# Kernel optimization log

Measured on AMD Instinct MI355X. Metric: run time of the kernel, lower is better.

The kernel has to match this reference:

```python
import jax, jax.numpy as jnp
import numpy as np

N_NODES = 50000


def _gcn_conv(x, W, b, src, dst, n):
    # PyG GCNConv: linear, then D^{-1/2}(A+I)D^{-1/2} aggregation, then bias.
    x = x @ W  # [N, out]
    loops = jnp.arange(n, dtype=src.dtype)
    src_f = jnp.concatenate([src, loops])  # add self-loops
    dst_f = jnp.concatenate([dst, loops])
    deg = jax.ops.segment_sum(jnp.ones_like(dst_f, dtype=x.dtype), dst_f, num_segments=n)
    dinv = jnp.where(deg > 0, jax.lax.rsqrt(deg), 0.0)
    norm = dinv[src_f] * dinv[dst_f]            # [E+N]
    msg = x[src_f] * norm[:, None]              # gather + scale
    out = jax.ops.segment_sum(msg, dst_f, num_segments=n)  # scatter-add
    return out + b


def setup_inputs() -> dict:
    key = jax.random.key(0)
    k1, k2, k3, k4 = jax.random.split(key, 4)
    ninp = 128
    emb = jax.random.normal(k1, (N_NODES, ninp), dtype=jnp.float32)
    emb = emb.at[0].set(0.0)  # padding_idx=0
    W1 = jax.random.normal(k2, (ninp, 2 * ninp), dtype=jnp.float32) * (1.0 / np.sqrt(ninp))
    b1 = jnp.zeros((2 * ninp,), dtype=jnp.float32)
    W2 = jax.random.normal(k3, (2 * ninp, ninp), dtype=jnp.float32) * (1.0 / np.sqrt(2 * ninp))
    b2 = jnp.zeros((ninp,), dtype=jnp.float32)
    edge_index = jax.random.randint(k4, (2, 800000), 0, N_NODES, dtype=jnp.int64)
    return {"emb": emb, "W1": W1, "b1": b1, "W2": W2, "b2": b2, "edge_index": edge_index}


def reference(emb, W1, b1, W2, b2, edge_index) -> jnp.ndarray:
    src, dst = edge_index[0], edge_index[1]
    h = _gcn_conv(emb, W1, b1, src, dst, N_NODES)   # [N, 2*ninp]
    # dropout in eval mode -> identity
    out = _gcn_conv(h, W2, b2, src, dst, N_NODES)   # [N, ninp]
    return out
```

## Files before the change

### kernel.cpp

```cpp
#include <hip/hip_runtime.h>

#define N_NODES 50000
#define N_EDGES 800000
#define NB 196

typedef unsigned int uint;
typedef short bf16x8 __attribute__((ext_vector_type(8)));
typedef float f32x4 __attribute__((ext_vector_type(4)));

__device__ __forceinline__ ushort f2bf(float f) {
    union { float f; uint u; } v; v.f = f;
    uint r = (v.u + 0x7FFFu + ((v.u >> 16) & 1u)) >> 16;
    return (ushort)r;
}
__device__ __forceinline__ float bf_lo(uint u) { return __uint_as_float(u << 16); }
__device__ __forceinline__ float bf_hi(uint u) { return __uint_as_float(u & 0xFFFF0000u); }

__global__ void k_tobf16(const float* __restrict__ in, uint* __restrict__ out) {
    int t = blockIdx.x * 256 + threadIdx.x;
    const float4* i4 = (const float4*)in + (size_t)t * 2;
    float4 v0 = i4[0], v1 = i4[1];
    uint4 o;
    o.x = (uint)f2bf(v0.x) | ((uint)f2bf(v0.y) << 16);
    o.y = (uint)f2bf(v0.z) | ((uint)f2bf(v0.w) << 16);
    o.z = (uint)f2bf(v1.x) | ((uint)f2bf(v1.y) << 16);
    o.w = (uint)f2bf(v1.z) | ((uint)f2bf(v1.w) << 16);
    ((uint4*)out)[t] = o;
}

__global__ void k_w12(const float* __restrict__ W1, const float* __restrict__ W2,
                      const float* __restrict__ b1, ushort* __restrict__ W12t,
                      float* __restrict__ bvec) {
    int n = threadIdx.x;
    int k = blockIdx.x;
    float s = 0.f;
    if (k < 128) {
        for (int m = 0; m < 256; ++m) s = fmaf(W1[(size_t)k * 256 + m], W2[(size_t)m * 128 + n], s);
        W12t[(size_t)n * 128 + k] = f2bf(s);
    } else {
        for (int m = 0; m < 256; ++m) s = fmaf(b1[m], W2[(size_t)m * 128 + n], s);
        bvec[n] = s;
    }
}


__global__ void k_zero(int* counts) {
    int i = blockIdx.x * 256 + threadIdx.x;
    if (i < N_NODES) counts[i] = 0;
}

__global__ void k_histrank(const int* __restrict__ dst, int* __restrict__ counts,
                           ushort* __restrict__ rank) {
    int e = blockIdx.x * 256 + threadIdx.x;
    if (e < N_EDGES) rank[e] = (ushort)atomicAdd(&counts[dst[e]], 1);
}

__global__ void k_blocksum(const int* __restrict__ counts, int* __restrict__ bsum) {
    __shared__ int lds[256];
    int t = threadIdx.x;
    int i = blockIdx.x * 256 + t;
    int v = (i < N_NODES) ? counts[i] : 0;
    lds[t] = v;
    __syncthreads();
    for (int off = 128; off > 0; off >>= 1) {
        if (t < off) lds[t] += lds[t + off];
        __syncthreads();
    }
    if (t == 0) bsum[blockIdx.x] = lds[0];
}

__global__ void k_scanb(const int* __restrict__ bsum, int* __restrict__ boff) {
    __shared__ int lds[256];
    int t = threadIdx.x;
    int v = (t < NB) ? bsum[t] : 0;
    lds[t] = v;
    __syncthreads();
    for (int off = 1; off < 256; off <<= 1) {
        int o = (t >= off) ? lds[t - off] : 0;
        __syncthreads();
        lds[t] += o;
        __syncthreads();
    }
    if (t < NB) boff[t] = lds[t] - v;
}

__global__ void k_scatter_rp(const int* __restrict__ counts, const int* __restrict__ boff,
                             int* __restrict__ row_ptr, float* __restrict__ dinv) {
    __shared__ int lds[256];
    int t = threadIdx.x;
    int i = blockIdx.x * 256 + t;
    int v = (i < N_NODES) ? counts[i] : 0;
    lds[t] = v;
    __syncthreads();
    for (int off = 1; off < 256; off <<= 1) {
        int o = (t >= off) ? lds[t - off] : 0;
        __syncthreads();
        lds[t] += o;
        __syncthreads();
    }
    if (i < N_NODES) {
        row_ptr[i] = boff[blockIdx.x] + lds[t] - v;
        dinv[i] = rsqrtf((float)(v + 1));
    }
    if (i == 0) row_ptr[N_NODES] = N_EDGES;
}

__global__ void k_fillr(const int* __restrict__ src, const int* __restrict__ dst,
                        const ushort* __restrict__ rank, const int* __restrict__ row_ptr,
                        ushort* __restrict__ csr_src) {
    int e = blockIdx.x * 256 + threadIdx.x;
    if (e >= N_EDGES) return;
    int pos = row_ptr[dst[e]] + (int)rank[e];
    csr_src[pos] = (ushort)src[e];
}

template<bool NVEC>
__global__ void k_gather128h(const uint* __restrict__ xh, const ushort* __restrict__ csr,
                             const int* __restrict__ rp, const float* __restrict__ dinv,
                             uint* __restrict__ outp, float* __restrict__ nvec) {
    int node = blockIdx.x * 4 + (threadIdx.x >> 6);
    int lane = threadIdx.x & 63;
    int q = lane >> 4;
    int fl = lane & 15;
    int beg = rp[node], end = rp[node + 1];
    const uint4* xb = (const uint4*)xh;
    float a[8];
    #pragma unroll
    for (int i = 0; i < 8; ++i) a[i] = 0.f;
    float sc = 0.f;

    for (int j = beg + q; j < end; j += 16) {
        int j1 = j + 4, j2 = j + 8, j3 = j + 12;
        int s0 = csr[j];
        int s1 = (j1 < end) ? (int)csr[j1] : s0;
        int s2 = (j2 < end) ? (int)csr[j2] : s0;
        int s3 = (j3 < end) ? (int)csr[j3] : s0;
        float c0 = dinv[s0];
        float c1 = (j1 < end) ? dinv[s1] : 0.f;
        float c2 = (j2 < end) ? dinv[s2] : 0.f;
        float c3 = (j3 < end) ? dinv[s3] : 0.f;
        uint4 u0 = xb[(size_t)s0 * 16 + fl];
        uint4 u1 = xb[(size_t)s1 * 16 + fl];
        uint4 u2 = xb[(size_t)s2 * 16 + fl];
        uint4 u3 = xb[(size_t)s3 * 16 + fl];
        sc += c0 + c1 + c2 + c3;
        a[0] = fmaf(c0, bf_lo(u0.x), a[0]); a[1] = fmaf(c0, bf_hi(u0.x), a[1]);
        a[2] = fmaf(c0, bf_lo(u0.y), a[2]); a[3] = fmaf(c0, bf_hi(u0.y), a[3]);
        a[4] = fmaf(c0, bf_lo(u0.z), a[4]); a[5] = fmaf(c0, bf_hi(u0.z), a[5]);
        a[6] = fmaf(c0, bf_lo(u0.w), a[6]); a[7] = fmaf(c0, bf_hi(u0.w), a[7]);
        a[0] = fmaf(c1, bf_lo(u1.x), a[0]); a[1] = fmaf(c1, bf_hi(u1.x), a[1]);
        a[2] = fmaf(c1, bf_lo(u1.y), a[2]); a[3] = fmaf(c1, bf_hi(u1.y), a[3]);
        a[4] = fmaf(c1, bf_lo(u1.z), a[4]); a[5] = fmaf(c1, bf_hi(u1.z), a[5]);
        a[6] = fmaf(c1, bf_lo(u1.w), a[6]); a[7] = fmaf(c1, bf_hi(u1.w), a[7]);
        a[0] = fmaf(c2, bf_lo(u2.x), a[0]); a[1] = fmaf(c2, bf_hi(u2.x), a[1]);
        a[2] = fmaf(c2, bf_lo(u2.y), a[2]); a[3] = fmaf(c2, bf_hi(u2.y), a[3]);
        a[4] = fmaf(c2, bf_lo(u2.z), a[4]); a[5] = fmaf(c2, bf_hi(u2.z), a[5]);
        a[6] = fmaf(c2, bf_lo(u2.w), a[6]); a[7] = fmaf(c2, bf_hi(u2.w), a[7]);
        a[0] = fmaf(c3, bf_lo(u3.x), a[0]); a[1] = fmaf(c3, bf_hi(u3.x), a[1]);
        a[2] = fmaf(c3, bf_lo(u3.y), a[2]); a[3] = fmaf(c3, bf_hi(u3.y), a[3]);
        a[4] = fmaf(c3, bf_lo(u3.z), a[4]); a[5] = fmaf(c3, bf_hi(u3.z), a[5]);
        a[6] = fmaf(c3, bf_lo(u3.w), a[6]); a[7] = fmaf(c3, bf_hi(u3.w), a[7]);
    }
    #pragma unroll
    for (int off = 16; off < 64; off <<= 1) {
        #pragma unroll
        for (int i = 0; i < 8; ++i) a[i] += __shfl_xor(a[i], off);
        sc += __shfl_xor(sc, off);
    }
    if (q == 0) {
        float dd = dinv[node];
        float dd2 = dd * dd;
        uint4 u = xb[(size_t)node * 16 + fl];
        float s[8] = { bf_lo(u.x), bf_hi(u.x), bf_lo(u.y), bf_hi(u.y),
                       bf_lo(u.z), bf_hi(u.z), bf_lo(u.w), bf_hi(u.w) };
        uint4 p;
        float o0 = fmaf(dd, a[0], dd2 * s[0]), o1 = fmaf(dd, a[1], dd2 * s[1]);
        float o2 = fmaf(dd, a[2], dd2 * s[2]), o3 = fmaf(dd, a[3], dd2 * s[3]);
        float o4 = fmaf(dd, a[4], dd2 * s[4]), o5 = fmaf(dd, a[5], dd2 * s[5]);
        float o6 = fmaf(dd, a[6], dd2 * s[6]), o7 = fmaf(dd, a[7], dd2 * s[7]);
        p.x = (uint)f2bf(o0) | ((uint)f2bf(o1) << 16);
        p.y = (uint)f2bf(o2) | ((uint)f2bf(o3) << 16);
        p.z = (uint)f2bf(o4) | ((uint)f2bf(o5) << 16);
        p.w = (uint)f2bf(o6) | ((uint)f2bf(o7) << 16);
        ((uint4*)outp)[(size_t)node * 16 + fl] = p;
        if (NVEC && fl == 0) nvec[node] = fmaf(dd, sc, dd2);
    }
}

__global__ void __launch_bounds__(256)
k_gemm_out(const ushort* __restrict__ A, const ushort* __restrict__ Wt,
           const float* __restrict__ nvec, const float* __restrict__ bvec,
           const float* __restrict__ b2, float* __restrict__ out) {
    constexpr int K = 128, NC = 128, KC = 4, TPW = 2;
    const int lane = threadIdx.x & 63;
    const int wave = threadIdx.x >> 6;
    const int row0 = blockIdx.x * 16;
    const int r = row0 + (lane & 15);
    const int ksub = (lane >> 4) * 8;

    f32x4 acc[TPW];
    int col[TPW];
    #pragma unroll
    for (int t = 0; t < TPW; ++t) {
        acc[t] = (f32x4){0.f, 0.f, 0.f, 0.f};
        col[t] = (wave * TPW + t) * 16 + (lane & 15);
    }
    #pragma unroll
    for (int kc = 0; kc < KC; ++kc) {
        bf16x8 af = *(const bf16x8*)(A + (size_t)r * K + kc * 32 + ksub);
        #pragma unroll
        for (int t = 0; t < TPW; ++t) {
            bf16x8 bf = *(const bf16x8*)(Wt + (size_t)col[t] * K + kc * 32 + ksub);
            acc[t] = __builtin_amdgcn_mfma_f32_16x16x32_bf16(af, bf, acc[t], 0, 0, 0);
        }
    }
    const int rb = row0 + (lane >> 4) * 4;
    float nv[4];
    #pragma unroll
    for (int e = 0; e < 4; ++e) nv[e] = nvec[rb + e];
    #pragma unroll
    for (int t = 0; t < TPW; ++t) {
        float bv = bvec[col[t]];
        float bb = b2[col[t]];
        #pragma unroll
        for (int e = 0; e < 4; ++e) {
            out[(size_t)(rb + e) * NC + col[t]] = acc[t][e] + nv[e] * bv + bb;
        }
    }
}

extern "C" void kernel_launch(void* const* d_in, const int* in_sizes, int n_in,
                              void* d_out, int out_size, void* d_ws, size_t ws_size,
                              hipStream_t stream) {
    const float* emb = (const float*)d_in[0];
    const float* W1  = (const float*)d_in[1];
    const float* b1  = (const float*)d_in[2];
    const float* W2  = (const float*)d_in[3];
    const float* b2  = (const float*)d_in[4];
    const int*   ei  = (const int*)d_in[5];
    const int* src = ei;
    const int* dst = ei + N_EDGES;

    char* ws = (char*)d_ws;
    float*  dinv    = (float*) (ws);
    int*    counts  = (int*)   (ws + (256ull << 10));
    int*    row_ptr = (int*)   (ws + (512ull << 10));
    int*    bsum    = (int*)   (ws + (768ull << 10));
    int*    boff    = (int*)   (ws + (772ull << 10));
    ushort* rank    = (ushort*)(ws + (1ull << 20));
    ushort* csr_src = (ushort*)(ws + (3ull << 20));
    ushort* W12t    = (ushort*)(ws + (5ull << 20));
    float*  bvec    = (float*) (ws + (5ull << 20) + (64ull << 10));
    float*  nvec    = (float*) (ws + (5ull << 20) + (128ull << 10));
    uint*   emb_h   = (uint*)  (ws + (6ull  << 20));
    uint*   G       = (uint*)  (ws + (19ull << 20));
    uint*   G2      = (uint*)  (ws + (32ull << 20));
    float*  out     = (float*)d_out;

    k_tobf16<<<N_NODES * 128 / 8 / 256, 256, 0, stream>>>(emb, emb_h);
    k_w12<<<129, 128, 0, stream>>>(W1, W2, b1, W12t, bvec);

    k_zero<<<NB, 256, 0, stream>>>(counts);
    k_histrank<<<(N_EDGES + 255) / 256, 256, 0, stream>>>(dst, counts, rank);
    k_blocksum<<<NB, 256, 0, stream>>>(counts, bsum);
    k_scanb<<<1, 256, 0, stream>>>(bsum, boff);
    k_scatter_rp<<<NB, 256, 0, stream>>>(counts, boff, row_ptr, dinv);
    k_fillr<<<(N_EDGES + 255) / 256, 256, 0, stream>>>(src, dst, rank, row_ptr, csr_src);

    k_gather128h<false><<<12500, 256, 0, stream>>>(emb_h, csr_src, row_ptr, dinv, G, nullptr);
    k_gather128h<true><<<12500, 256, 0, stream>>>(G, csr_src, row_ptr, dinv, G2, nvec);
    k_gemm_out<<<N_NODES / 16, 256, 0, stream>>>((const ushort*)G2, W12t, nvec, bvec, b2, out);
}
```

Baseline: 159.9 us.

## Split bf16 features into 16-column chunks and gather each chunk separately

```diff
diff --git a/kernel.cpp b/kernel.cpp
--- a/kernel.cpp
+++ b/kernel.cpp
@@ -16,8 +16,9 @@
 __device__ __forceinline__ float bf_lo(uint u) { return __uint_as_float(u << 16); }
 __device__ __forceinline__ float bf_hi(uint u) { return __uint_as_float(u & 0xFFFF0000u); }
 
-__global__ void k_tobf16(const float* __restrict__ in, uint* __restrict__ out) {
+__global__ void k_tobf16c(const float* __restrict__ in, uint* __restrict__ out) {
     int t = blockIdx.x * 256 + threadIdx.x;
+    int node = t >> 4, part = t & 15;
     const float4* i4 = (const float4*)in + (size_t)t * 2;
     float4 v0 = i4[0], v1 = i4[1];
     uint4 o;
@@ -25,7 +26,8 @@
     o.y = (uint)f2bf(v0.z) | ((uint)f2bf(v0.w) << 16);
     o.z = (uint)f2bf(v1.x) | ((uint)f2bf(v1.y) << 16);
     o.w = (uint)f2bf(v1.z) | ((uint)f2bf(v1.w) << 16);
-    ((uint4*)out)[t] = o;
+    int c8 = part >> 1, half = part & 1;
+    ((uint4*)out)[((size_t)c8 * N_NODES + node) * 2 + half] = o;
 }
 
 __global__ void k_w12(const float* __restrict__ W1, const float* __restrict__ W2,
@@ -115,75 +117,45 @@
 }
 
 template<bool NVEC>
-__global__ void k_gather128h(const uint* __restrict__ xh, const ushort* __restrict__ csr,
-                             const int* __restrict__ rp, const float* __restrict__ dinv,
-                             uint* __restrict__ outp, float* __restrict__ nvec) {
-    int node = blockIdx.x * 4 + (threadIdx.x >> 6);
+__global__ void k_gatherc(const uint* __restrict__ xh, const ushort* __restrict__ csr,
+                          const int* __restrict__ rp, const float* __restrict__ dinv,
+                          uint* __restrict__ outp, float* __restrict__ nvec) {
+    int b = blockIdx.x;
+    int c = b & 7;
+    int node = (b >> 3) * 4 + (threadIdx.x >> 6);
     int lane = threadIdx.x & 63;
-    int q = lane >> 4;
-    int fl = lane & 15;
+    int g = lane >> 3, fl = lane & 7;
     int beg = rp[node], end = rp[node + 1];
-    const uint4* xb = (const uint4*)xh;
-    float a[8];
-    #pragma unroll
-    for (int i = 0; i < 8; ++i) a[i] = 0.f;
-    float sc = 0.f;
-
-    for (int j = beg + q; j < end; j += 16) {
-        int j1 = j + 4, j2 = j + 8, j3 = j + 12;
+    const uint* tb = xh + (size_t)c * N_NODES * 8;
+    float a0 = 0.f, a1 = 0.f, sc = 0.f;
+
+    for (int j = beg + g; j < end; j += 16) {
         int s0 = csr[j];
+        float c0 = dinv[s0];
+        uint u0 = tb[(size_t)s0 * 8 + fl];
+        int j1 = j + 8;
         int s1 = (j1 < end) ? (int)csr[j1] : s0;
-        int s2 = (j2 < end) ? (int)csr[j2] : s0;
-        int s3 = (j3 < end) ? (int)csr[j3] : s0;
-        float c0 = dinv[s0];
         float c1 = (j1 < end) ? dinv[s1] : 0.f;
-        float c2 = (j2 < end) ? dinv[s2] : 0.f;
-        float c3 = (j3 < end) ? dinv[s3] : 0.f;
-        uint4 u0 = xb[(size_t)s0 * 16 + fl];
-        uint4 u1 = xb[(size_t)s1 * 16 + fl];
-        uint4 u2 = xb[(size_t)s2 * 16 + fl];
-        uint4 u3 = xb[(size_t)s3 * 16 + fl];
-        sc += c0 + c1 + c2 + c3;
-        a[0] = fmaf(c0, bf_lo(u0.x), a[0]); a[1] = fmaf(c0, bf_hi(u0.x), a[1]);
-        a[2] = fmaf(c0, bf_lo(u0.y), a[2]); a[3] = fmaf(c0, bf_hi(u0.y), a[3]);
-        a[4] = fmaf(c0, bf_lo(u0.z), a[4]); a[5] = fmaf(c0, bf_hi(u0.z), a[5]);
-        a[6] = fmaf(c0, bf_lo(u0.w), a[6]); a[7] = fmaf(c0, bf_hi(u0.w), a[7]);
-        a[0] = fmaf(c1, bf_lo(u1.x), a[0]); a[1] = fmaf(c1, bf_hi(u1.x), a[1]);
-        a[2] = fmaf(c1, bf_lo(u1.y), a[2]); a[3] = fmaf(c1, bf_hi(u1.y), a[3]);
-        a[4] = fmaf(c1, bf_lo(u1.z), a[4]); a[5] = fmaf(c1, bf_hi(u1.z), a[5]);
-        a[6] = fmaf(c1, bf_lo(u1.w), a[6]); a[7] = fmaf(c1, bf_hi(u1.w), a[7]);
-        a[0] = fmaf(c2, bf_lo(u2.x), a[0]); a[1] = fmaf(c2, bf_hi(u2.x), a[1]);
-        a[2] = fmaf(c2, bf_lo(u2.y), a[2]); a[3] = fmaf(c2, bf_hi(u2.y), a[3]);
-        a[4] = fmaf(c2, bf_lo(u2.z), a[4]); a[5] = fmaf(c2, bf_hi(u2.z), a[5]);
-        a[6] = fmaf(c2, bf_lo(u2.w), a[6]); a[7] = fmaf(c2, bf_hi(u2.w), a[7]);
-        a[0] = fmaf(c3, bf_lo(u3.x), a[0]); a[1] = fmaf(c3, bf_hi(u3.x), a[1]);
-        a[2] = fmaf(c3, bf_lo(u3.y), a[2]); a[3] = fmaf(c3, bf_hi(u3.y), a[3]);
-        a[4] = fmaf(c3, bf_lo(u3.z), a[4]); a[5] = fmaf(c3, bf_hi(u3.z), a[5]);
-        a[6] = fmaf(c3, bf_lo(u3.w), a[6]); a[7] = fmaf(c3, bf_hi(u3.w), a[7]);
-    }
-    #pragma unroll
-    for (int off = 16; off < 64; off <<= 1) {
-        #pragma unroll
-        for (int i = 0; i < 8; ++i) a[i] += __shfl_xor(a[i], off);
-        sc += __shfl_xor(sc, off);
-    }
-    if (q == 0) {
+        uint u1 = tb[(size_t)s1 * 8 + fl];
+        sc += c0 + c1;
+        a0 = fmaf(c0, bf_lo(u0), a0); a1 = fmaf(c0, bf_hi(u0), a1);
+        a0 = fmaf(c1, bf_lo(u1), a0); a1 = fmaf(c1, bf_hi(u1), a1);
+    }
+    #pragma unroll
+    for (int off = 8; off < 64; off <<= 1) {
+        a0 += __shfl_xor(a0, off);
+        a1 += __shfl_xor(a1, off);
+        if (NVEC) sc += __shfl_xor(sc, off);
+    }
+    if (g == 0) {
         float dd = dinv[node];
         float dd2 = dd * dd;
-        uint4 u = xb[(size_t)node * 16 + fl];
-        float s[8] = { bf_lo(u.x), bf_hi(u.x), bf_lo(u.y), bf_hi(u.y),
-                       bf_lo(u.z), bf_hi(u.z), bf_lo(u.w), bf_hi(u.w) };
-        uint4 p;
-        float o0 = fmaf(dd, a[0], dd2 * s[0]), o1 = fmaf(dd, a[1], dd2 * s[1]);
-        float o2 = fmaf(dd, a[2], dd2 * s[2]), o3 = fmaf(dd, a[3], dd2 * s[3]);
-        float o4 = fmaf(dd, a[4], dd2 * s[4]), o5 = fmaf(dd, a[5], dd2 * s[5]);
-        float o6 = fmaf(dd, a[6], dd2 * s[6]), o7 = fmaf(dd, a[7], dd2 * s[7]);
-        p.x = (uint)f2bf(o0) | ((uint)f2bf(o1) << 16);
-        p.y = (uint)f2bf(o2) | ((uint)f2bf(o3) << 16);
-        p.z = (uint)f2bf(o4) | ((uint)f2bf(o5) << 16);
-        p.w = (uint)f2bf(o6) | ((uint)f2bf(o7) << 16);
-        ((uint4*)outp)[(size_t)node * 16 + fl] = p;
-        if (NVEC && fl == 0) nvec[node] = fmaf(dd, sc, dd2);
+        uint u = tb[(size_t)node * 8 + fl];
+        float o0 = fmaf(dd, a0, dd2 * bf_lo(u));
+        float o1 = fmaf(dd, a1, dd2 * bf_hi(u));
+        uint p = (uint)f2bf(o0) | ((uint)f2bf(o1) << 16);
+        __builtin_nontemporal_store(p, &outp[((size_t)c * N_NODES + node) * 8 + fl]);
+        if (NVEC && c == 0 && fl == 0) nvec[node] = fmaf(dd, sc, dd2);
     }
 }
 
@@ -207,7 +179,8 @@
     }
     #pragma unroll
     for (int kc = 0; kc < KC; ++kc) {
-        bf16x8 af = *(const bf16x8*)(A + (size_t)r * K + kc * 32 + ksub);
+        int c8 = kc * 2 + (ksub >> 4);
+        bf16x8 af = *(const bf16x8*)(A + ((size_t)c8 * N_NODES + r) * 16 + (ksub & 15));
         #pragma unroll
         for (int t = 0; t < TPW; ++t) {
             bf16x8 bf = *(const bf16x8*)(Wt + (size_t)col[t] * K + kc * 32 + ksub);
@@ -257,7 +230,7 @@
     uint*   G2      = (uint*)  (ws + (32ull << 20));
     float*  out     = (float*)d_out;
 
-    k_tobf16<<<N_NODES * 128 / 8 / 256, 256, 0, stream>>>(emb, emb_h);
+    k_tobf16c<<<N_NODES * 16 / 256, 256, 0, stream>>>(emb, emb_h);
     k_w12<<<129, 128, 0, stream>>>(W1, W2, b1, W12t, bvec);
 
     k_zero<<<NB, 256, 0, stream>>>(counts);
@@ -267,7 +240,7 @@
     k_scatter_rp<<<NB, 256, 0, stream>>>(counts, boff, row_ptr, dinv);
     k_fillr<<<(N_EDGES + 255) / 256, 256, 0, stream>>>(src, dst, rank, row_ptr, csr_src);
 
-    k_gather128h<false><<<12500, 256, 0, stream>>>(emb_h, csr_src, row_ptr, dinv, G, nullptr);
-    k_gather128h<true><<<12500, 256, 0, stream>>>(G, csr_src, row_ptr, dinv, G2, nvec);
+    k_gatherc<false><<<(N_NODES / 4) * 8, 256, 0, stream>>>(emb_h, csr_src, row_ptr, dinv, G, nullptr);
+    k_gatherc<true><<<(N_NODES / 4) * 8, 256, 0, stream>>>(G, csr_src, row_ptr, dinv, G2, nvec);
     k_gemm_out<<<N_NODES / 16, 256, 0, stream>>>((const ushort*)G2, W12t, nvec, bvec, b2, out);
 }
```

Result: slower. 295.4 us (+84.7%).
